# Optimization experiments

Hardware: AMD Instinct MI355X
Metric: run time of the kernel (lower is better)

## Reference

```python
import jax, jax.numpy as jnp
import numpy as np

E = 768
H_HEADS = 12


def trilinear_border_sample(feat_map, coords):
    """grid_sample 3D, mode='bilinear', padding_mode='border', align_corners=True.
    feat_map: (B, C, D, H, W); coords: (B, P, 3) in [-1,1], last dim = (x, y, z) -> (W, H, D).
    Returns (B, P, C).
    """
    B, C, D, H, W = feat_map.shape
    x, y, z = coords[..., 0], coords[..., 1], coords[..., 2]
    ix = (x + 1.0) * 0.5 * (W - 1)
    iy = (y + 1.0) * 0.5 * (H - 1)
    iz = (z + 1.0) * 0.5 * (D - 1)
    x0 = jnp.floor(ix); y0 = jnp.floor(iy); z0 = jnp.floor(iz)
    wx = ix - x0; wy = iy - y0; wz = iz - z0
    x0i = jnp.clip(x0, 0, W - 1).astype(jnp.int32)
    x1i = jnp.clip(x0 + 1, 0, W - 1).astype(jnp.int32)
    y0i = jnp.clip(y0, 0, H - 1).astype(jnp.int32)
    y1i = jnp.clip(y0 + 1, 0, H - 1).astype(jnp.int32)
    z0i = jnp.clip(z0, 0, D - 1).astype(jnp.int32)
    z1i = jnp.clip(z0 + 1, 0, D - 1).astype(jnp.int32)
    flat = feat_map.reshape(B, C, D * H * W)

    def gather(zi, yi, xi):
        idx = (zi * H + yi) * W + xi  # (B, P)
        return jnp.take_along_axis(flat, idx[:, None, :], axis=2)  # (B, C, P)

    out = (
        gather(z0i, y0i, x0i) * ((1 - wz) * (1 - wy) * (1 - wx))[:, None, :]
        + gather(z0i, y0i, x1i) * ((1 - wz) * (1 - wy) * wx)[:, None, :]
        + gather(z0i, y1i, x0i) * ((1 - wz) * wy * (1 - wx))[:, None, :]
        + gather(z0i, y1i, x1i) * ((1 - wz) * wy * wx)[:, None, :]
        + gather(z1i, y0i, x0i) * (wz * (1 - wy) * (1 - wx))[:, None, :]
        + gather(z1i, y0i, x1i) * (wz * (1 - wy) * wx)[:, None, :]
        + gather(z1i, y1i, x0i) * (wz * wy * (1 - wx))[:, None, :]
        + gather(z1i, y1i, x1i) * (wz * wy * wx)[:, None, :]
    )
    return out.transpose(0, 2, 1)  # (B, P, C)


def setup_inputs() -> dict:
    key = jax.random.key(0)
    ks = jax.random.split(key, 12)
    B, fullN, nb = 64, 513, 32
    s = 1.0 / np.sqrt(E)
    return {
        "x": jax.random.normal(ks[0], (B, fullN, E), jnp.float32),
        "bio_embed": jax.random.normal(ks[1], (B, E), jnp.float32),
        "base_coords": jax.random.uniform(ks[2], (nb, 3), jnp.float32),
        "offsets": jax.random.normal(ks[3], (B, nb, 3), jnp.float32) * 0.1,
        "confidence": jax.random.uniform(ks[4], (B, 1), jnp.float32),
        "sample_proj_w": jax.random.uniform(ks[5], (E, E), jnp.float32, -s, s),
        "sample_proj_b": jax.random.uniform(ks[6], (E,), jnp.float32, -s, s),
        "in_proj_w": jax.random.uniform(ks[7], (3 * E, E), jnp.float32, -s, s),
        "in_proj_b": jnp.zeros((3 * E,), jnp.float32),
        "out_proj_w": jax.random.uniform(ks[8], (E, E), jnp.float32, -s, s),
        "out_proj_b": jnp.zeros((E,), jnp.float32),
        "grid_size": 8,
    }


def reference(x, bio_embed, base_coords, offsets, confidence,
              sample_proj_w, sample_proj_b, in_proj_w, in_proj_b,
              out_proj_w, out_proj_b, grid_size):
    B, fullN, C = x.shape
    G = grid_size
    patch_tokens = x[:, 1:, :]  # (B, N, C), N = G^3
    feat_map = patch_tokens.transpose(0, 2, 1).reshape(B, C, G, G, G)

    coords = jnp.clip(base_coords[None, :, :] + offsets, -1.0, 1.0)  # (B, nb, 3)
    sampled = trilinear_border_sample(feat_map, coords)  # (B, nb, C)
    sampled = sampled @ sample_proj_w.T + sample_proj_b

    # MultiheadAttention: single query (bio_embed), keys/values = sampled tokens
    hd = E // H_HEADS
    Wq, Wk, Wv = in_proj_w[:E], in_proj_w[E:2 * E], in_proj_w[2 * E:]
    bq, bk, bv = in_proj_b[:E], in_proj_b[E:2 * E], in_proj_b[2 * E:]
    q = (bio_embed @ Wq.T + bq).reshape(B, H_HEADS, hd)
    k = (sampled @ Wk.T + bk).reshape(B, -1, H_HEADS, hd)
    v = (sampled @ Wv.T + bv).reshape(B, -1, H_HEADS, hd)
    scores = jnp.einsum('bhd,bphd->bhp', q, k) / jnp.sqrt(jnp.asarray(hd, q.dtype))
    attn = jax.nn.softmax(scores, axis=-1)
    ctx = jnp.einsum('bhp,bphd->bhd', attn, v).reshape(B, E)
    attn_out = ctx @ out_proj_w.T + out_proj_b  # (B, E)

    out = jnp.broadcast_to(attn_out[:, None, :], (B, fullN, C))
    out = out * confidence[:, :, None]
    return out
```

## Files before the change

kernel.cpp:

```cpp
#include <hip/hip_runtime.h>
#include <hip/hip_bf16.h>
#include <math.h>

#define E 768
#define NH 12
#define HD 64
#define NTHR 256
#define SLICES 8

typedef __attribute__((ext_vector_type(8))) short bf16x8;
typedef __attribute__((ext_vector_type(4))) float f32x4;

__device__ __forceinline__ unsigned short f2bf_rne(float f) {
    unsigned int u = __float_as_uint(f);
    u += 0x7FFF + ((u >> 16) & 1);
    return (unsigned short)(u >> 16);
}

__device__ __forceinline__ float bf2f(unsigned short u) {
    return __uint_as_float((unsigned)u << 16);
}

__device__ __forceinline__ void sample_one(
    const float* x, const float* bcrd, const float* offs, int G,
    unsigned short* sampled, int u, int P, int fullN, int t, int tstep)
{
    int b = u / P, p = u % P;
    float gm1 = (float)(G - 1);

    float cx = bcrd[p * 3 + 0] + offs[u * 3 + 0];
    float cy = bcrd[p * 3 + 1] + offs[u * 3 + 1];
    float cz = bcrd[p * 3 + 2] + offs[u * 3 + 2];
    cx = fminf(fmaxf(cx, -1.f), 1.f);
    cy = fminf(fmaxf(cy, -1.f), 1.f);
    cz = fminf(fmaxf(cz, -1.f), 1.f);

    float ix = (cx + 1.f) * 0.5f * gm1;
    float iy = (cy + 1.f) * 0.5f * gm1;
    float iz = (cz + 1.f) * 0.5f * gm1;
    float fx = floorf(ix), fy = floorf(iy), fz = floorf(iz);
    float wx = ix - fx, wy = iy - fy, wz = iz - fz;

    int x0 = (int)fminf(fmaxf(fx,       0.f), gm1);
    int x1 = (int)fminf(fmaxf(fx + 1.f, 0.f), gm1);
    int y0 = (int)fminf(fmaxf(fy,       0.f), gm1);
    int y1 = (int)fminf(fmaxf(fy + 1.f, 0.f), gm1);
    int z0 = (int)fminf(fmaxf(fz,       0.f), gm1);
    int z1 = (int)fminf(fmaxf(fz + 1.f, 0.f), gm1);

    int tk[8];
    tk[0] = (z0 * G + y0) * G + x0;
    tk[1] = (z0 * G + y0) * G + x1;
    tk[2] = (z0 * G + y1) * G + x0;
    tk[3] = (z0 * G + y1) * G + x1;
    tk[4] = (z1 * G + y0) * G + x0;
    tk[5] = (z1 * G + y0) * G + x1;
    tk[6] = (z1 * G + y1) * G + x0;
    tk[7] = (z1 * G + y1) * G + x1;
    float wgt[8];
    wgt[0] = (1.f - wz) * (1.f - wy) * (1.f - wx);
    wgt[1] = (1.f - wz) * (1.f - wy) * wx;
    wgt[2] = (1.f - wz) * wy * (1.f - wx);
    wgt[3] = (1.f - wz) * wy * wx;
    wgt[4] = wz * (1.f - wy) * (1.f - wx);
    wgt[5] = wz * (1.f - wy) * wx;
    wgt[6] = wz * wy * (1.f - wx);
    wgt[7] = wz * wy * wx;

    const float4* xb4 = (const float4*)(x + ((size_t)b * fullN + 1) * E);
    ushort4* outp = (ushort4*)(sampled + (size_t)u * E);
    for (int c4 = t; c4 < E / 4; c4 += tstep) {
        float4 acc = {0.f, 0.f, 0.f, 0.f};
#pragma unroll
        for (int k = 0; k < 8; ++k) {
            float4 v = xb4[(size_t)tk[k] * (E / 4) + c4];
            acc.x += wgt[k] * v.x; acc.y += wgt[k] * v.y;
            acc.z += wgt[k] * v.z; acc.w += wgt[k] * v.w;
        }
        ushort4 o;
        o.x = f2bf_rne(acc.x); o.y = f2bf_rne(acc.y);
        o.z = f2bf_rne(acc.z); o.w = f2bf_rne(acc.w);
        outp[c4] = o;
    }
}

__device__ __forceinline__ void w2_tile(
    const float* Wkv, const float* spw, unsigned short* w2_bf,
    int n0, int k0, unsigned short* lsA, unsigned short* lsB)
{
    int t = threadIdx.x;
    int wv = t >> 6;
    int ln = t & 63;
    int wm = (wv & 1) * 32;
    int wn = (wv >> 1) * 32;

    f32x4 acc[2][2] = {};

    for (int j0 = 0; j0 < E; j0 += 32) {
#pragma unroll
        for (int rep = 0; rep < 2; ++rep) {
            int fi = t + rep * 256;
            int r = fi >> 3, c4 = fi & 7;
            float4 v = *(const float4*)(Wkv + (size_t)(n0 + r) * E + j0 + c4 * 4);
            ushort4 o;
            o.x = f2bf_rne(v.x); o.y = f2bf_rne(v.y);
            o.z = f2bf_rne(v.z); o.w = f2bf_rne(v.w);
            *(ushort4*)(lsA + r * 32 + c4 * 4) = o;
        }
#pragma unroll
        for (int rep = 0; rep < 2; ++rep) {
            int fi = t + rep * 256;
            int kk = fi >> 3, j4 = fi & 7;
            const float* sp = spw + (size_t)(j0 + j4 * 4) * E + k0 + kk;
            ushort4 o;
            o.x = f2bf_rne(sp[0 * E]);
            o.y = f2bf_rne(sp[1 * E]);
            o.z = f2bf_rne(sp[2 * E]);
            o.w = f2bf_rne(sp[3 * E]);
            *(ushort4*)(lsB + kk * 32 + j4 * 4) = o;
        }
        __syncthreads();

        int kq = (ln >> 4) * 8;
        int rsel = ln & 15;
        bf16x8 af[2], bfr[2];
#pragma unroll
        for (int i = 0; i < 2; ++i) {
            af[i]  = *(const bf16x8*)&lsA[(wm + i * 16 + rsel) * 32 + kq];
            bfr[i] = *(const bf16x8*)&lsB[(wn + i * 16 + rsel) * 32 + kq];
        }
#pragma unroll
        for (int i = 0; i < 2; ++i)
#pragma unroll
            for (int j = 0; j < 2; ++j)
                acc[i][j] = __builtin_amdgcn_mfma_f32_16x16x32_bf16(
                    af[i], bfr[j], acc[i][j], 0, 0, 0);
        __syncthreads();
    }

    int cr = (ln >> 4) * 4;
    int cc = ln & 15;
#pragma unroll
    for (int j = 0; j < 2; ++j) {
        int col = k0 + wn + j * 16 + cc;
#pragma unroll
        for (int i = 0; i < 2; ++i) {
#pragma unroll
            for (int r = 0; r < 4; ++r) {
                int row = n0 + wm + i * 16 + cr + r;
                w2_bf[(size_t)row * E + col] = f2bf_rne(acc[i][j][r]);
            }
        }
    }
}

__device__ __forceinline__ void matvec_wave_v4(
    const float* A, const float* W, const float* bias, float* C,
    int u, int N, int ln)
{
    int m = u / N, n = u % N;
    const float4* a4 = (const float4*)(A + (size_t)m * E);
    const float4* w4 = (const float4*)(W + (size_t)n * E);
    float s = 0.f;
#pragma unroll
    for (int j = 0; j < 3; ++j) {
        float4 av = a4[ln + 64 * j];
        float4 wv = w4[ln + 64 * j];
        s += av.x * wv.x + av.y * wv.y + av.z * wv.z + av.w * wv.w;
    }
#pragma unroll
    for (int off = 32; off; off >>= 1) s += __shfl_down(s, off);
    if (ln == 0) C[u] = s + bias[n];
}

__global__ __launch_bounds__(256) void prep_kernel(
    const float* __restrict__ x,
    const float* __restrict__ bcrd, const float* __restrict__ offs,
    const int* __restrict__ gsize,
    const float* __restrict__ bio,
    const float* __restrict__ spw, const float* __restrict__ spb,
    const float* __restrict__ ipw, const float* __restrict__ ipb,
    unsigned short* __restrict__ sampled_bf, unsigned short* __restrict__ w2_bf,
    float* __restrict__ q, float* __restrict__ b2,
    int B, int P, int fullN, int nb_sample, int nb_w2, int nb_q)
{
    __shared__ unsigned short lsA[64 * 32];
    __shared__ unsigned short lsB[64 * 32];

    int blk = blockIdx.x;
    int t = threadIdx.x;
    int wv = t >> 6, ln = t & 63;
    const float* Wkv = ipw + (size_t)E * E;

    if (blk < nb_sample) {
        sample_one(x, bcrd, offs, *gsize, sampled_bf, blk, P, fullN, t, NTHR);
        return;
    }
    blk -= nb_sample;
    if (blk < nb_w2) {
        w2_tile(Wkv, spw, w2_bf, (blk / 12) * 64, (blk % 12) * 64, lsA, lsB);
        return;
    }
    blk -= nb_w2;
    if (blk < nb_q) {
        int u = blk * 4 + wv;
        if (u < B * E) matvec_wave_v4(bio, ipw, ipb, q, u, E, ln);
        return;
    }
    blk -= nb_q;
    {
        int u = blk * 4 + wv;
        if (u < 2 * E) matvec_wave_v4(spb, Wkv, ipb + E, b2, u, 2 * E, ln);
    }
}

__global__ __launch_bounds__(256) void attn_ctx(
    const float* __restrict__ q, const unsigned short* __restrict__ sampled_bf,
    const unsigned short* __restrict__ w2_bf, const float* __restrict__ b2,
    float* __restrict__ ctx, int B, int P)
{
    __shared__ float q_lds[HD];
    __shared__ __align__(16) float u_lds[E];
    __shared__ float sc_lds[64];
    __shared__ float at_lds[64];
    __shared__ __align__(16) float cx_lds[E];

    int b = blockIdx.x % B;
    int h = blockIdx.x / B;
    int t = threadIdx.x, wv = t >> 6, ln = t & 63;

    const unsigned short* W2k = w2_bf + (size_t)(h * HD) * E;
    const unsigned short* W2v = w2_bf + (size_t)(E + h * HD) * E;
    const unsigned short* smp = sampled_bf + (size_t)(b * P) * E;

    if (t < HD) q_lds[t] = q[(size_t)b * E + h * HD + t];
    __syncthreads();

    if (t < E / 4) {
        float4 uu = {0.f, 0.f, 0.f, 0.f};
        for (int d = 0; d < HD; ++d) {
            float qd = q_lds[d];
            ushort4 r = *(const ushort4*)(W2k + (size_t)d * E + 4 * t);
            uu.x += qd * bf2f(r.x); uu.y += qd * bf2f(r.y);
            uu.z += qd * bf2f(r.z); uu.w += qd * bf2f(r.w);
        }
        *(float4*)&u_lds[4 * t] = uu;
    }
    __syncthreads();

    for (int p = wv; p < P; p += 4) {
        const unsigned short* sr = smp + (size_t)p * E;
        float s = 0.f;
#pragma unroll
        for (int c = 0; c < E / 64; ++c)
            s += u_lds[ln + 64 * c] * bf2f(sr[ln + 64 * c]);
#pragma unroll
        for (int off = 32; off; off >>= 1) s += __shfl_xor(s, off);
        if (ln == 0) sc_lds[p] = s * 0.125f;
    }
    __syncthreads();

    if (wv == 0) {
        float s = (ln < P) ? sc_lds[ln] : -INFINITY;
        float mx = s;
#pragma unroll
        for (int off = 32; off; off >>= 1) mx = fmaxf(mx, __shfl_xor(mx, off));
        float ex = (ln < P) ? __expf(s - mx) : 0.f;
        float den = ex;
#pragma unroll
        for (int off = 32; off; off >>= 1) den += __shfl_xor(den, off);
        if (ln < P) at_lds[ln] = ex / den;
    }
    __syncthreads();

    if (t < E / 4) {
        float4 cc = {0.f, 0.f, 0.f, 0.f};
        for (int p = 0; p < P; ++p) {
            float a = at_lds[p];
            ushort4 r = *(const ushort4*)(smp + (size_t)p * E + 4 * t);
            cc.x += a * bf2f(r.x); cc.y += a * bf2f(r.y);
            cc.z += a * bf2f(r.z); cc.w += a * bf2f(r.w);
        }
        *(float4*)&cx_lds[4 * t] = cc;
    }
    __syncthreads();

    for (int d = wv; d < HD; d += 4) {
        const unsigned short* vr = W2v + (size_t)d * E;
        float s = 0.f;
#pragma unroll
        for (int c = 0; c < E / 64; ++c)
            s += cx_lds[ln + 64 * c] * bf2f(vr[ln + 64 * c]);
#pragma unroll
        for (int off = 32; off; off >>= 1) s += __shfl_down(s, off);
        if (ln == 0)
            ctx[(size_t)b * E + h * HD + d] = s + b2[E + h * HD + d];
    }
}

__global__ __launch_bounds__(256) void outproj_kernel(
    const float* __restrict__ ctx, const float* __restrict__ opw,
    const float* __restrict__ opb, float* __restrict__ aout, int B)
{
    __shared__ __align__(16) float ctx_lds[E];

    int b = blockIdx.x % B;
    int g = blockIdx.x / B;
    int t = threadIdx.x, wv = t >> 6, ln = t & 63;

    for (int i = t; i < E; i += NTHR) ctx_lds[i] = ctx[(size_t)b * E + i];
    __syncthreads();

    const float4* c4p = (const float4*)ctx_lds;
#pragma unroll 2
    for (int idx = 0; idx < 24; ++idx) {
        int n = g * 96 + wv * 24 + idx;
        const float4* w4 = (const float4*)(opw + (size_t)n * E);
        float s = 0.f;
#pragma unroll
        for (int j = 0; j < 3; ++j) {
            float4 wvv = w4[ln + 64 * j];
            float4 cv = c4p[ln + 64 * j];
            s += wvv.x * cv.x + wvv.y * cv.y + wvv.z * cv.z + wvv.w * cv.w;
        }
#pragma unroll
        for (int off = 32; off; off >>= 1) s += __shfl_down(s, off);
        if (ln == 0) aout[(size_t)b * E + n] = s + opb[n];
    }
}

__global__ void bcast_kernel(const float* __restrict__ attn_out,
                             const float* __restrict__ conf,
                             float* __restrict__ out,
                             int fullN, int pc)
{
    int b = blockIdx.y;
    float cf = conf[b];
    const float4* ao = (const float4*)(attn_out + (size_t)b * E);
    float4* ob = (float4*)(out + (size_t)b * fullN * E);
    int i = blockIdx.x * blockDim.x + threadIdx.x;
    if (i < pc) {
        int c4 = i % (E / 4);
        float4 v = ao[c4];
        v.x *= cf; v.y *= cf; v.z *= cf; v.w *= cf;
        ob[i] = v;
    }
}

extern "C" void kernel_launch(void* const* d_in, const int* in_sizes, int n_in,
                              void* d_out, int out_size, void* d_ws, size_t ws_size,
                              hipStream_t stream)
{
    const float* x      = (const float*)d_in[0];
    const float* bio    = (const float*)d_in[1];
    const float* bcrd   = (const float*)d_in[2];
    const float* offs   = (const float*)d_in[3];
    const float* conf   = (const float*)d_in[4];
    const float* spw    = (const float*)d_in[5];
    const float* spb    = (const float*)d_in[6];
    const float* ipw    = (const float*)d_in[7];
    const float* ipb    = (const float*)d_in[8];
    const float* opw    = (const float*)d_in[9];
    const float* opb    = (const float*)d_in[10];
    const int*   gsize  = (const int*)d_in[11];
    float* out = (float*)d_out;

    int B     = in_sizes[1] / E;
    int P     = in_sizes[2] / 3;
    int fullN = in_sizes[0] / (B * E);
    int M     = B * P;

    char* base = (char*)d_out;
    unsigned short* sampled_bf = (unsigned short*)(base + 0);
    unsigned short* w2_bf      = (unsigned short*)(base + 3145728);

    float* q    = (float*)d_ws;
    float* b2   = (float*)((char*)d_ws + 196608);
    float* ctx  = (float*)((char*)d_ws + 262144);
    float* aout = (float*)((char*)d_ws + 524288);

    int nb_sample = M;
    int nb_w2     = (2 * E / 64) * (E / 64);
    int nb_q      = (B * E + 3) / 4;
    int nb_b2     = (2 * E + 3) / 4;
    prep_kernel<<<nb_sample + nb_w2 + nb_q + nb_b2, NTHR, 0, stream>>>(
        x, bcrd, offs, gsize, bio, spw, spb, ipw, ipb,
        sampled_bf, w2_bf, q, b2, B, P, fullN, nb_sample, nb_w2, nb_q);

    attn_ctx<<<B * NH, NTHR, 0, stream>>>(q, sampled_bf, w2_bf, b2, ctx, B, P);

    outproj_kernel<<<B * SLICES, NTHR, 0, stream>>>(ctx, opw, opb, aout, B);

    int pc = fullN * E / 4;
    bcast_kernel<<<dim3((pc + 255) / 256, B), NTHR, 0, stream>>>(
        aout, conf, out, fullN, pc);
}
```

Before: 270.5 us.

## Fuse attention heads and output projection into one per-batch kernel

Merges the per-head attention kernel and the separate output-projection kernel into a single kernel with one block per batch, looping over all 12 heads and then applying the output projection from a transposed weight. The transposed out-projection weight is built in the prep kernel, written into spare output-buffer space. This removes a kernel launch and the ctx round-trip through global memory. In exchange, parallelism drops from B*12 blocks to B blocks (64), which serialises the per-head work and may leave most compute units idle.

```diff
diff --git a/kernel.cpp b/kernel.cpp
--- a/kernel.cpp
+++ b/kernel.cpp
@@ -6,7 +6,6 @@
 #define NH 12
 #define HD 64
 #define NTHR 256
-#define SLICES 8
 
 typedef __attribute__((ext_vector_type(8))) short bf16x8;
 typedef __attribute__((ext_vector_type(4))) float f32x4;
@@ -173,6 +172,26 @@
     if (ln == 0) C[u] = s + bias[n];
 }
 
+__device__ __forceinline__ void transpose_tile(
+    const float* opw, float* opwT, int n0, int k0)
+{
+    __shared__ float ts[64][65];
+    int t = threadIdx.x;
+#pragma unroll
+    for (int rep = 0; rep < 16; ++rep) {
+        int idx = t + rep * 256;
+        int r = idx >> 6, c = idx & 63;
+        ts[r][c] = opw[(size_t)(n0 + r) * E + k0 + c];
+    }
+    __syncthreads();
+#pragma unroll
+    for (int rep = 0; rep < 16; ++rep) {
+        int idx = t + rep * 256;
+        int r = idx >> 6, c = idx & 63;
+        opwT[(size_t)(k0 + r) * E + n0 + c] = ts[c][r];
+    }
+}
+
 __global__ __launch_bounds__(256) void prep_kernel(
     const float* __restrict__ x,
     const float* __restrict__ bcrd, const float* __restrict__ offs,
@@ -180,9 +199,10 @@
     const float* __restrict__ bio,
     const float* __restrict__ spw, const float* __restrict__ spb,
     const float* __restrict__ ipw, const float* __restrict__ ipb,
+    const float* __restrict__ opw,
     unsigned short* __restrict__ sampled_bf, unsigned short* __restrict__ w2_bf,
-    float* __restrict__ q, float* __restrict__ b2,
-    int B, int P, int fullN, int nb_sample, int nb_w2, int nb_q)
+    float* __restrict__ q, float* __restrict__ b2, float* __restrict__ opwT,
+    int B, int P, int fullN, int nb_sample, int nb_w2, int nb_q, int nb_b2)
 {
     __shared__ unsigned short lsA[64 * 32];
     __shared__ unsigned short lsB[64 * 32];
@@ -208,124 +228,124 @@
         return;
     }
     blk -= nb_q;
-    {
+    if (blk < nb_b2) {
         int u = blk * 4 + wv;
         if (u < 2 * E) matvec_wave_v4(spb, Wkv, ipb + E, b2, u, 2 * E, ln);
-    }
-}
-
-__global__ __launch_bounds__(256) void attn_ctx(
+        return;
+    }
+    blk -= nb_b2;
+    {
+        transpose_tile(opw, opwT, (blk % 12) * 64, (blk / 12) * 64);
+    }
+}
+
+__global__ __launch_bounds__(256) void attn_full(
     const float* __restrict__ q, const unsigned short* __restrict__ sampled_bf,
     const unsigned short* __restrict__ w2_bf, const float* __restrict__ b2,
-    float* __restrict__ ctx, int B, int P)
-{
-    __shared__ float q_lds[HD];
+    const float* __restrict__ opwT, const float* __restrict__ opb,
+    float* __restrict__ aout, int B, int P)
+{
+    __shared__ __align__(16) float q_lds[E];
     __shared__ __align__(16) float u_lds[E];
     __shared__ float sc_lds[64];
     __shared__ float at_lds[64];
-    __shared__ __align__(16) float cx_lds[E];
-
-    int b = blockIdx.x % B;
-    int h = blockIdx.x / B;
+    __shared__ __align__(16) float cs_lds[E];
+    __shared__ __align__(16) float ctx_lds[E];
+
+    int b = blockIdx.x;
     int t = threadIdx.x, wv = t >> 6, ln = t & 63;
 
-    const unsigned short* W2k = w2_bf + (size_t)(h * HD) * E;
-    const unsigned short* W2v = w2_bf + (size_t)(E + h * HD) * E;
     const unsigned short* smp = sampled_bf + (size_t)(b * P) * E;
 
-    if (t < HD) q_lds[t] = q[(size_t)b * E + h * HD + t];
+    for (int i = t; i < E; i += NTHR) q_lds[i] = q[(size_t)b * E + i];
     __syncthreads();
 
+    for (int h = 0; h < NH; ++h) {
+        const unsigned short* W2k = w2_bf + (size_t)(h * HD) * E;
+        const unsigned short* W2v = w2_bf + (size_t)(E + h * HD) * E;
+        const float* qh = q_lds + h * HD;
+
+        if (t < E / 4) {
+            float4 uu = {0.f, 0.f, 0.f, 0.f};
+            for (int d = 0; d < HD; ++d) {
+                float qd = qh[d];
+                ushort4 r = *(const ushort4*)(W2k + (size_t)d * E + 4 * t);
+                uu.x += qd * bf2f(r.x); uu.y += qd * bf2f(r.y);
+                uu.z += qd * bf2f(r.z); uu.w += qd * bf2f(r.w);
+            }
+            *(float4*)&u_lds[4 * t] = uu;
+        }
+        __syncthreads();
+
+        for (int p = wv; p < P; p += 4) {
+            const unsigned short* sr = smp + (size_t)p * E;
+            float s = 0.f;
+#pragma unroll
+            for (int c = 0; c < E / 64; ++c)
+                s += u_lds[ln + 64 * c] * bf2f(sr[ln + 64 * c]);
+#pragma unroll
+            for (int off = 32; off; off >>= 1) s += __shfl_xor(s, off);
+            if (ln == 0) sc_lds[p] = s * 0.125f;
+        }
+        __syncthreads();
+
+        if (wv == 0) {
+            float s = (ln < P) ? sc_lds[ln] : -INFINITY;
+            float mx = s;
+#pragma unroll
+            for (int off = 32; off; off >>= 1) mx = fmaxf(mx, __shfl_xor(mx, off));
+            float ex = (ln < P) ? __expf(s - mx) : 0.f;
+            float den = ex;
+#pragma unroll
+            for (int off = 32; off; off >>= 1) den += __shfl_xor(den, off);
+            if (ln < P) at_lds[ln] = ex / den;
+        }
+        __syncthreads();
+
+        if (t < E / 4) {
+            float4 cc = {0.f, 0.f, 0.f, 0.f};
+            for (int p = 0; p < P; ++p) {
+                float a = at_lds[p];
+                ushort4 r = *(const ushort4*)(smp + (size_t)p * E + 4 * t);
+                cc.x += a * bf2f(r.x); cc.y += a * bf2f(r.y);
+                cc.z += a * bf2f(r.z); cc.w += a * bf2f(r.w);
+            }
+            *(float4*)&cs_lds[4 * t] = cc;
+        }
+        __syncthreads();
+
+        for (int d = wv; d < HD; d += 4) {
+            const unsigned short* vr = W2v + (size_t)d * E;
+            float s = 0.f;
+#pragma unroll
+            for (int c = 0; c < E / 64; ++c)
+                s += cs_lds[ln + 64 * c] * bf2f(vr[ln + 64 * c]);
+#pragma unroll
+            for (int off = 32; off; off >>= 1) s += __shfl_down(s, off);
+            if (ln == 0)
+                ctx_lds[h * HD + d] = s + b2[E + h * HD + d];
+        }
+        __syncthreads();
+    }
+
     if (t < E / 4) {
-        float4 uu = {0.f, 0.f, 0.f, 0.f};
-        for (int d = 0; d < HD; ++d) {
-            float qd = q_lds[d];
-            ushort4 r = *(const ushort4*)(W2k + (size_t)d * E + 4 * t);
-            uu.x += qd * bf2f(r.x); uu.y += qd * bf2f(r.y);
-            uu.z += qd * bf2f(r.z); uu.w += qd * bf2f(r.w);
-        }
-        *(float4*)&u_lds[4 * t] = uu;
-    }
-    __syncthreads();
-
-    for (int p = wv; p < P; p += 4) {
-        const unsigned short* sr = smp + (size_t)p * E;
-        float s = 0.f;
-#pragma unroll
-        for (int c = 0; c < E / 64; ++c)
-            s += u_lds[ln + 64 * c] * bf2f(sr[ln + 64 * c]);
-#pragma unroll
-        for (int off = 32; off; off >>= 1) s += __shfl_xor(s, off);
-        if (ln == 0) sc_lds[p] = s * 0.125f;
-    }
-    __syncthreads();
-
-    if (wv == 0) {
-        float s = (ln < P) ? sc_lds[ln] : -INFINITY;
-        float mx = s;
-#pragma unroll
-        for (int off = 32; off; off >>= 1) mx = fmaxf(mx, __shfl_xor(mx, off));
-        float ex = (ln < P) ? __expf(s - mx) : 0.f;
-        float den = ex;
-#pragma unroll
-        for (int off = 32; off; off >>= 1) den += __shfl_xor(den, off);
-        if (ln < P) at_lds[ln] = ex / den;
-    }
-    __syncthreads();
-
-    if (t < E / 4) {
-        float4 cc = {0.f, 0.f, 0.f, 0.f};
-        for (int p = 0; p < P; ++p) {
-            float a = at_lds[p];
-            ushort4 r = *(const ushort4*)(smp + (size_t)p * E + 4 * t);
-            cc.x += a * bf2f(r.x); cc.y += a * bf2f(r.y);
-            cc.z += a * bf2f(r.z); cc.w += a * bf2f(r.w);
-        }
-        *(float4*)&cx_lds[4 * t] = cc;
-    }
-    __syncthreads();
-
-    for (int d = wv; d < HD; d += 4) {
-        const unsigned short* vr = W2v + (size_t)d * E;
-        float s = 0.f;
-#pragma unroll
-        for (int c = 0; c < E / 64; ++c)
-            s += cx_lds[ln + 64 * c] * bf2f(vr[ln + 64 * c]);
-#pragma unroll
-        for (int off = 32; off; off >>= 1) s += __shfl_down(s, off);
-        if (ln == 0)
-            ctx[(size_t)b * E + h * HD + d] = s + b2[E + h * HD + d];
-    }
-}
-
-__global__ __launch_bounds__(256) void outproj_kernel(
-    const float* __restrict__ ctx, const float* __restrict__ opw,
-    const float* __restrict__ opb, float* __restrict__ aout, int B)
-{
-    __shared__ __align__(16) float ctx_lds[E];
-
-    int b = blockIdx.x % B;
-    int g = blockIdx.x / B;
-    int t = threadIdx.x, wv = t >> 6, ln = t & 63;
-
-    for (int i = t; i < E; i += NTHR) ctx_lds[i] = ctx[(size_t)b * E + i];
-    __syncthreads();
-
-    const float4* c4p = (const float4*)ctx_lds;
-#pragma unroll 2
-    for (int idx = 0; idx < 24; ++idx) {
-        int n = g * 96 + wv * 24 + idx;
-        const float4* w4 = (const float4*)(opw + (size_t)n * E);
-        float s = 0.f;
-#pragma unroll
-        for (int j = 0; j < 3; ++j) {
-            float4 wvv = w4[ln + 64 * j];
-            float4 cv = c4p[ln + 64 * j];
-            s += wvv.x * cv.x + wvv.y * cv.y + wvv.z * cv.z + wvv.w * cv.w;
-        }
-#pragma unroll
-        for (int off = 32; off; off >>= 1) s += __shfl_down(s, off);
-        if (ln == 0) aout[(size_t)b * E + n] = s + opb[n];
+        f32x4 a0 = {0.f, 0.f, 0.f, 0.f};
+        f32x4 a1 = {0.f, 0.f, 0.f, 0.f};
+        f32x4 a2 = {0.f, 0.f, 0.f, 0.f};
+        f32x4 a3 = {0.f, 0.f, 0.f, 0.f};
+        for (int k = 0; k < E; k += 4) {
+            float c0 = ctx_lds[k + 0], c1 = ctx_lds[k + 1];
+            float c2 = ctx_lds[k + 2], c3 = ctx_lds[k + 3];
+            f32x4 w0 = *(const f32x4*)(opwT + (size_t)(k + 0) * E + 4 * t);
+            f32x4 w1 = *(const f32x4*)(opwT + (size_t)(k + 1) * E + 4 * t);
+            f32x4 w2 = *(const f32x4*)(opwT + (size_t)(k + 2) * E + 4 * t);
+            f32x4 w3 = *(const f32x4*)(opwT + (size_t)(k + 3) * E + 4 * t);
+            a0 += c0 * w0; a1 += c1 * w1; a2 += c2 * w2; a3 += c3 * w3;
+        }
+        f32x4 s = (a0 + a1) + (a2 + a3);
+        f32x4 bb = *(const f32x4*)(opb + 4 * t);
+        s += bb;
+        *(f32x4*)(aout + (size_t)b * E + 4 * t) = s;
     }
 }
 
@@ -373,23 +393,24 @@
     char* base = (char*)d_out;
     unsigned short* sampled_bf = (unsigned short*)(base + 0);
     unsigned short* w2_bf      = (unsigned short*)(base + 3145728);
+    float*          opwT       = (float*)(base + 5505024);
 
     float* q    = (float*)d_ws;
     float* b2   = (float*)((char*)d_ws + 196608);
-    float* ctx  = (float*)((char*)d_ws + 262144);
-    float* aout = (float*)((char*)d_ws + 524288);
+    float* aout = (float*)((char*)d_ws + 262144);
 
     int nb_sample = M;
     int nb_w2     = (2 * E / 64) * (E / 64);
     int nb_q      = (B * E + 3) / 4;
     int nb_b2     = (2 * E + 3) / 4;
-    prep_kernel<<<nb_sample + nb_w2 + nb_q + nb_b2, NTHR, 0, stream>>>(
-        x, bcrd, offs, gsize, bio, spw, spb, ipw, ipb,
-        sampled_bf, w2_bf, q, b2, B, P, fullN, nb_sample, nb_w2, nb_q);
-
-    attn_ctx<<<B * NH, NTHR, 0, stream>>>(q, sampled_bf, w2_bf, b2, ctx, B, P);
-
-    outproj_kernel<<<B * SLICES, NTHR, 0, stream>>>(ctx, opw, opb, aout, B);
+    int nb_T      = 12 * 12;
+    prep_kernel<<<nb_sample + nb_w2 + nb_q + nb_b2 + nb_T, NTHR, 0, stream>>>(
+        x, bcrd, offs, gsize, bio, spw, spb, ipw, ipb, opw,
+        sampled_bf, w2_bf, q, b2, opwT,
+        B, P, fullN, nb_sample, nb_w2, nb_q, nb_b2);
+
+    attn_full<<<B, NTHR, 0, stream>>>(q, sampled_bf, w2_bf, b2, opwT, opb,
+                                      aout, B, P);
 
     int pc = fullN * E / 4;
     bcast_kernel<<<dim3((pc + 255) / 256, B), NTHR, 0, stream>>>(
```

New measurement: 476.6 us. 1.76x slower.

## Fuse out-projection into attention kernel via per-head atomic accumulation

Applied to the files above, without the earlier changes.

Removes the separate out-projection kernel. Each attention block now multiplies its head's 64-dim context slice by the matching columns of the out-projection weight and atomically adds the partial result into the output. The prep kernel pre-fills that output with the out-projection bias. The sample-projection weight tile load is also changed to coalesced float4 row reads with a transposed scatter into LDS. This saves one launch and the ctx round trip, but adds atomics and strided weight reads per head, and the scalar LDS stores may cause bank conflicts.

```diff
diff --git a/kernel.cpp b/kernel.cpp
--- a/kernel.cpp
+++ b/kernel.cpp
@@ -6,7 +6,6 @@
 #define NH 12
 #define HD 64
 #define NTHR 256
-#define SLICES 8
 
 typedef __attribute__((ext_vector_type(8))) short bf16x8;
 typedef __attribute__((ext_vector_type(4))) float f32x4;
@@ -107,17 +106,20 @@
             o.z = f2bf_rne(v.z); o.w = f2bf_rne(v.w);
             *(ushort4*)(lsA + r * 32 + c4 * 4) = o;
         }
-#pragma unroll
-        for (int rep = 0; rep < 2; ++rep) {
-            int fi = t + rep * 256;
-            int kk = fi >> 3, j4 = fi & 7;
-            const float* sp = spw + (size_t)(j0 + j4 * 4) * E + k0 + kk;
-            ushort4 o;
-            o.x = f2bf_rne(sp[0 * E]);
-            o.y = f2bf_rne(sp[1 * E]);
-            o.z = f2bf_rne(sp[2 * E]);
-            o.w = f2bf_rne(sp[3 * E]);
-            *(ushort4*)(lsB + kk * 32 + j4 * 4) = o;
+        {
+            int r = t >> 3, c8 = t & 7;
+            const float* sp = spw + (size_t)(j0 + r) * E + k0 + c8 * 8;
+            float4 v0 = *(const float4*)(sp);
+            float4 v1 = *(const float4*)(sp + 4);
+            int kb = c8 * 8;
+            lsB[(kb + 0) * 32 + r] = f2bf_rne(v0.x);
+            lsB[(kb + 1) * 32 + r] = f2bf_rne(v0.y);
+            lsB[(kb + 2) * 32 + r] = f2bf_rne(v0.z);
+            lsB[(kb + 3) * 32 + r] = f2bf_rne(v0.w);
+            lsB[(kb + 4) * 32 + r] = f2bf_rne(v1.x);
+            lsB[(kb + 5) * 32 + r] = f2bf_rne(v1.y);
+            lsB[(kb + 6) * 32 + r] = f2bf_rne(v1.z);
+            lsB[(kb + 7) * 32 + r] = f2bf_rne(v1.w);
         }
         __syncthreads();
 
@@ -180,9 +182,10 @@
     const float* __restrict__ bio,
     const float* __restrict__ spw, const float* __restrict__ spb,
     const float* __restrict__ ipw, const float* __restrict__ ipb,
+    const float* __restrict__ opb,
     unsigned short* __restrict__ sampled_bf, unsigned short* __restrict__ w2_bf,
-    float* __restrict__ q, float* __restrict__ b2,
-    int B, int P, int fullN, int nb_sample, int nb_w2, int nb_q)
+    float* __restrict__ q, float* __restrict__ b2, float* __restrict__ aout,
+    int B, int P, int fullN, int nb_sample, int nb_w2, int nb_q, int nb_b2)
 {
     __shared__ unsigned short lsA[64 * 32];
     __shared__ unsigned short lsB[64 * 32];
@@ -208,22 +211,30 @@
         return;
     }
     blk -= nb_q;
-    {
+    if (blk < nb_b2) {
         int u = blk * 4 + wv;
         if (u < 2 * E) matvec_wave_v4(spb, Wkv, ipb + E, b2, u, 2 * E, ln);
-    }
-}
-
-__global__ __launch_bounds__(256) void attn_ctx(
+        return;
+    }
+    blk -= nb_b2;
+    {
+        int i = blk * NTHR + t;
+        float4 bb = ((const float4*)opb)[i % (E / 4)];
+        ((float4*)aout)[i] = bb;
+    }
+}
+
+__global__ __launch_bounds__(256) void attn_ctx_op(
     const float* __restrict__ q, const unsigned short* __restrict__ sampled_bf,
     const unsigned short* __restrict__ w2_bf, const float* __restrict__ b2,
-    float* __restrict__ ctx, int B, int P)
+    const float* __restrict__ opw, float* __restrict__ aout, int B, int P)
 {
     __shared__ float q_lds[HD];
     __shared__ __align__(16) float u_lds[E];
     __shared__ float sc_lds[64];
     __shared__ float at_lds[64];
     __shared__ __align__(16) float cx_lds[E];
+    __shared__ float ch_lds[HD];
 
     int b = blockIdx.x % B;
     int h = blockIdx.x / B;
@@ -293,39 +304,22 @@
             s += cx_lds[ln + 64 * c] * bf2f(vr[ln + 64 * c]);
 #pragma unroll
         for (int off = 32; off; off >>= 1) s += __shfl_down(s, off);
-        if (ln == 0)
-            ctx[(size_t)b * E + h * HD + d] = s + b2[E + h * HD + d];
-    }
-}
-
-__global__ __launch_bounds__(256) void outproj_kernel(
-    const float* __restrict__ ctx, const float* __restrict__ opw,
-    const float* __restrict__ opb, float* __restrict__ aout, int B)
-{
-    __shared__ __align__(16) float ctx_lds[E];
-
-    int b = blockIdx.x % B;
-    int g = blockIdx.x / B;
-    int t = threadIdx.x, wv = t >> 6, ln = t & 63;
-
-    for (int i = t; i < E; i += NTHR) ctx_lds[i] = ctx[(size_t)b * E + i];
-    __syncthreads();
-
-    const float4* c4p = (const float4*)ctx_lds;
-#pragma unroll 2
-    for (int idx = 0; idx < 24; ++idx) {
-        int n = g * 96 + wv * 24 + idx;
-        const float4* w4 = (const float4*)(opw + (size_t)n * E);
-        float s = 0.f;
-#pragma unroll
-        for (int j = 0; j < 3; ++j) {
-            float4 wvv = w4[ln + 64 * j];
-            float4 cv = c4p[ln + 64 * j];
-            s += wvv.x * cv.x + wvv.y * cv.y + wvv.z * cv.z + wvv.w * cv.w;
-        }
-#pragma unroll
-        for (int off = 32; off; off >>= 1) s += __shfl_down(s, off);
-        if (ln == 0) aout[(size_t)b * E + n] = s + opb[n];
+        if (ln == 0) ch_lds[d] = s + b2[E + h * HD + d];
+    }
+    __syncthreads();
+
+#pragma unroll
+    for (int jj = 0; jj < 3; ++jj) {
+        int n = t + jj * NTHR;
+        const float4* wr = (const float4*)(opw + (size_t)n * E + h * HD);
+        float acc = 0.f;
+#pragma unroll
+        for (int c = 0; c < HD / 4; ++c) {
+            float4 w = wr[c];
+            acc += w.x * ch_lds[4 * c] + w.y * ch_lds[4 * c + 1]
+                 + w.z * ch_lds[4 * c + 2] + w.w * ch_lds[4 * c + 3];
+        }
+        atomicAdd(&aout[(size_t)b * E + n], acc);
     }
 }
 
@@ -376,20 +370,20 @@
 
     float* q    = (float*)d_ws;
     float* b2   = (float*)((char*)d_ws + 196608);
-    float* ctx  = (float*)((char*)d_ws + 262144);
-    float* aout = (float*)((char*)d_ws + 524288);
+    float* aout = (float*)((char*)d_ws + 262144);
 
     int nb_sample = M;
     int nb_w2     = (2 * E / 64) * (E / 64);
     int nb_q      = (B * E + 3) / 4;
     int nb_b2     = (2 * E + 3) / 4;
-    prep_kernel<<<nb_sample + nb_w2 + nb_q + nb_b2, NTHR, 0, stream>>>(
-        x, bcrd, offs, gsize, bio, spw, spb, ipw, ipb,
-        sampled_bf, w2_bf, q, b2, B, P, fullN, nb_sample, nb_w2, nb_q);
-
-    attn_ctx<<<B * NH, NTHR, 0, stream>>>(q, sampled_bf, w2_bf, b2, ctx, B, P);
-
-    outproj_kernel<<<B * SLICES, NTHR, 0, stream>>>(ctx, opw, opb, aout, B);
+    int nb_ai     = (B * E / 4) / NTHR;
+    prep_kernel<<<nb_sample + nb_w2 + nb_q + nb_b2 + nb_ai, NTHR, 0, stream>>>(
+        x, bcrd, offs, gsize, bio, spw, spb, ipw, ipb, opb,
+        sampled_bf, w2_bf, q, b2, aout,
+        B, P, fullN, nb_sample, nb_w2, nb_q, nb_b2);
+
+    attn_ctx_op<<<B * NH, NTHR, 0, stream>>>(q, sampled_bf, w2_bf, b2,
+                                             opw, aout, B, P);
 
     int pc = fullN * E / 4;
     bcast_kernel<<<dim3((pc + 255) / 256, B), NTHR, 0, stream>>>(
```

Result: faster. 261.2 us (-3.4%).
